# Performance work log

Measured on AMD Instinct MI355X. Metric: run time of the kernel, lower is better.

Reference implementation:

```python
import jax, jax.numpy as jnp
import numpy as np

HEADS = 16
DIM_HEAD = 64
NONCAUSAL_ATTN_LEN = 64


def setup_inputs() -> dict:
    key = jax.random.key(0)
    k1, k2, k3 = jax.random.split(key, 3)
    b, n, d = 2, 2048, 1024
    inner = HEADS * DIM_HEAD
    x = jax.random.normal(k1, (b, n, d), dtype=jnp.float32)
    mask = jnp.ones((b, n), dtype=bool)
    w_qkv = jax.random.normal(k2, (d, 3 * inner), dtype=jnp.float32) * 0.02
    w_out = jax.random.normal(k3, (inner, d), dtype=jnp.float32) * 0.02
    b_out = jnp.zeros((d,), dtype=jnp.float32)
    return {"x": x, "mask": mask, "w_qkv": w_qkv, "w_out": w_out, "b_out": b_out}


def reference(x, mask, w_qkv, w_out, b_out):
    b, n, _ = x.shape
    h, dh = HEADS, DIM_HEAD
    scale = dh ** -0.5
    qkv = x @ w_qkv                                  # [b, n, 3*h*dh]
    q, k, v = jnp.split(qkv, 3, axis=-1)
    # 'b n (h d) -> b h n d'
    reshape = lambda t: t.reshape(b, n, h, dh).transpose(0, 2, 1, 3)
    q, k, v = reshape(q), reshape(k), reshape(v)
    dots = jnp.einsum('bhid,bhjd->bhij', q, k) * scale  # [b,h,n,n]
    neg = -jnp.finfo(dots.dtype).max
    # padding mask: attend only where both query and key positions are valid
    pm = mask[:, None, :, None] & mask[:, None, None, :]
    dots = jnp.where(~pm, neg, dots)
    # causal mask (strict upper triangle), with noncausal prefix block unmasked
    cm = jnp.triu(jnp.ones((n, n), dtype=bool), k=1)
    L = NONCAUSAL_ATTN_LEN
    if L > 1:
        cm = cm.at[:L, :L].set(False)
    dots = jnp.where(cm, neg, dots)
    attn = jax.nn.softmax(dots, axis=-1)
    out = jnp.einsum('bhij,bhjd->bhid', attn, v)     # [b,h,n,dh]
    out = out.transpose(0, 2, 1, 3).reshape(b, n, h * dh)  # 'b h n d -> b n (h d)'
    return out @ w_out + b_out
```

## Files before the change

kernel.cpp:

```cpp
#include <hip/hip_runtime.h>

typedef __bf16 bf16x8 __attribute__((ext_vector_type(8)));
typedef __bf16 bf16x4 __attribute__((ext_vector_type(4)));
typedef float  f32x4  __attribute__((ext_vector_type(4)));

#define SC2 0.18033688011112042f

__device__ __forceinline__ void gload16(const void* g, void* l) {
    __builtin_amdgcn_global_load_lds(
        (const __attribute__((address_space(1))) unsigned int*)g,
        (__attribute__((address_space(3))) unsigned int*)l, 16, 0, 0);
}

__device__ __forceinline__ float max3f(float a, float b, float c) {
    return fmaxf(fmaxf(a, b), c);
}

__global__ __launch_bounds__(256) void prep_k(
    const float* __restrict__ x, const float* __restrict__ w_qkv,
    const float* __restrict__ w_out, __bf16* __restrict__ xb,
    __bf16* __restrict__ wqkvT, __bf16* __restrict__ woutT)
{
    __shared__ float tile[32][33];
    const int blk = blockIdx.x, tid = threadIdx.x;
    if (blk < 4096) {
        int i = blk * 256 + tid;
        float4 v = ((const float4*)x)[i];
        bf16x4 o;
        o[0] = (__bf16)v.x; o[1] = (__bf16)v.y; o[2] = (__bf16)v.z; o[3] = (__bf16)v.w;
        ((bf16x4*)xb)[i] = o;
        return;
    }
    const float* in; __bf16* outp; int C, t0;
    if (blk < 7168) { in = w_qkv; outp = wqkvT; C = 3072; t0 = blk - 4096; }
    else            { in = w_out; outp = woutT; C = 1024; t0 = blk - 7168; }
    const int R = 1024;
    const int tpr = C >> 5;
    const int c0 = (t0 % tpr) * 32, r0 = (t0 / tpr) * 32;
    const int tx = tid & 31, ty = tid >> 5;
#pragma unroll
    for (int p = 0; p < 4; ++p)
        tile[ty + p * 8][tx] = in[(size_t)(r0 + ty + p * 8) * C + c0 + tx];
    __syncthreads();
#pragma unroll
    for (int p = 0; p < 4; ++p)
        outp[(size_t)(c0 + ty + p * 8) * R + r0 + tx] = (__bf16)tile[tx][ty + p * 8];
}

template<int MODE, int BM>
__global__ __launch_bounds__(256) void gemm_bf16_k(
    const __bf16* __restrict__ A, const __bf16* __restrict__ Bt,
    void* __restrict__ Cout, const float* __restrict__ bias,
    int M, int N, int K)
{
    constexpr int MI = BM / 32;
    constexpr int MPX = (BM == 128) ? 4 : 8;
    constexpr int MSH = (BM == 128) ? 2 : 3;
    __shared__ __bf16 As[2][BM * 32];
    __shared__ __bf16 Bs[2][128 * 32];
    const int tid = threadIdx.x;
    const int flat = blockIdx.y * gridDim.x + blockIdx.x;
    const int xcd = flat & 7, q = flat >> 3;
    const int mi = xcd * MPX + (q & (MPX - 1));
    const int ni = q >> MSH;
    const int m0 = mi * BM, n0 = ni * 128;
    const int wave = tid >> 6, lane = tid & 63;
    const int lr = lane & 15, lk = lane >> 4;

    const int row4 = lane >> 2;
    const int sg   = (lane & 3) ^ (row4 & 3);

    const int wm = (BM == 128) ? (wave >> 1) * 64 : (wave & 1) * 32;
    const int wn = (BM == 128) ? (wave & 1) * 64 : (wave >> 1) * 64;

    f32x4 acc[MI][4] = {};

    auto stage = [&](int k0, int bufi) {
        if (BM == 128) {
#pragma unroll
            for (int c = 0; c < 2; ++c) {
                int row = c * 64 + wave * 16 + row4;
                gload16(A + (size_t)(m0 + row) * K + k0 + sg * 8,
                        (char*)&As[bufi][0] + c * 4096 + wave * 1024);
            }
        } else {
            int row = wave * 16 + row4;
            gload16(A + (size_t)(m0 + row) * K + k0 + sg * 8,
                    (char*)&As[bufi][0] + wave * 1024);
        }
#pragma unroll
        for (int c = 0; c < 2; ++c) {
            int row = c * 64 + wave * 16 + row4;
            gload16(Bt + (size_t)(n0 + row) * K + k0 + sg * 8,
                    (char*)&Bs[bufi][0] + c * 4096 + wave * 1024);
        }
    };

    const int nsteps = K >> 5;
    stage(0, 0);
    for (int s = 0; s < nsteps; ++s) {
        __syncthreads();
        if (s + 1 < nsteps) stage((s + 1) * 32, (s + 1) & 1);
        const int bufi = s & 1;

        bf16x8 af[MI], bfr[4];
#pragma unroll
        for (int i = 0; i < MI; ++i) {
            int row = wm + i * 16 + lr;
            af[i]  = *(const bf16x8*)((char*)&As[bufi][0] + row * 64 +
                                      ((lk ^ (row & 3)) << 4));
        }
#pragma unroll
        for (int j = 0; j < 4; ++j) {
            int row = wn + j * 16 + lr;
            bfr[j] = *(const bf16x8*)((char*)&Bs[bufi][0] + row * 64 +
                                      ((lk ^ (row & 3)) << 4));
        }
        __builtin_amdgcn_s_setprio(1);
#pragma unroll
        for (int i = 0; i < MI; ++i)
#pragma unroll
            for (int j = 0; j < 4; ++j)
                acc[i][j] = __builtin_amdgcn_mfma_f32_16x16x32_bf16(
                    af[i], bfr[j], acc[i][j], 0, 0, 0);
        __builtin_amdgcn_s_setprio(0);
    }

#pragma unroll
    for (int i = 0; i < MI; ++i) {
#pragma unroll
        for (int j = 0; j < 4; ++j) {
            int row0 = m0 + wm + i * 16 + lk * 4;
            int col  = n0 + wn + j * 16 + lr;
            if (MODE == 0) {
                int which = col >> 10, rem = col & 1023;
                int h = rem >> 6, dh = rem & 63;
                int bb = row0 >> 11, nn0 = row0 & 2047;
                if (which == 2) {
                    bf16x4 o;
#pragma unroll
                    for (int r = 0; r < 4; ++r) o[r] = (__bf16)acc[i][j][r];
                    size_t off = (size_t)8388608 +
                                 (((size_t)bb * 16 + h) * 64 + dh) * 2048 + nn0;
                    *(bf16x4*)((__bf16*)Cout + off) = o;
                } else {
                    float sc = (which == 0) ? SC2 : 1.f;
#pragma unroll
                    for (int r = 0; r < 4; ++r) {
                        size_t off = ((((size_t)which * 2 + bb) * 16 + h) * 2048
                                      + nn0 + r) * 64 + dh;
                        ((__bf16*)Cout)[off] = (__bf16)(acc[i][j][r] * sc);
                    }
                }
            } else {
#pragma unroll
                for (int r = 0; r < 4; ++r)
                    ((float*)Cout)[(size_t)(row0 + r) * N + col] =
                        acc[i][j][r] + bias[col];
            }
        }
    }
}

__global__ __launch_bounds__(256) void flash_attn_k(
    const __bf16* __restrict__ qkv, __bf16* __restrict__ out)
{
    __shared__ __bf16 Ks[2][64 * 64];
    __shared__ __bf16 Vt[2][64 * 64];
    __shared__ __bf16 Ps[4 * 16 * 64];

    const int g = blockIdx.x;
    const int xcd = g & 7, i = g >> 3;
    const int bh = xcd + 8 * (i & 3);
    const int qp = i >> 2;
    const int qtA = qp, qtB = 31 - qp;
    const int b = bh >> 4, h = bh & 15;
    const int wave = threadIdx.x >> 6, lane = threadIdx.x & 63;
    const int lr = lane & 15, lk = lane >> 4;

    const size_t headoff = ((size_t)b * 16 + h) * 2048 * 64;
    const __bf16* Qp  = qkv + headoff;
    const __bf16* Kp  = qkv + (size_t)4194304 + headoff;
    const __bf16* Vtp = qkv + (size_t)8388608 + headoff;

    const int row8 = lane >> 3;
    const int sg   = (lane & 7) ^ row8;

    bf16x8 qfA[2], qfB[2];
    {
        const __bf16* qa = Qp + (size_t)(qtA * 64 + wave * 16 + lr) * 64 + lk * 8;
        qfA[0] = *(const bf16x8*)(qa);
        qfA[1] = *(const bf16x8*)(qa + 32);
        const __bf16* qb = Qp + (size_t)(qtB * 64 + wave * 16 + lr) * 64 + lk * 8;
        qfB[0] = *(const bf16x8*)(qb);
        qfB[1] = *(const bf16x8*)(qb + 32);
    }

    bf16x8 ones;
#pragma unroll
    for (int j = 0; j < 8; ++j) ones[j] = (__bf16)1.0f;

    float mA = 0.f, mB = 0.f;
    f32x4 lAacc = {}, lBacc = {};
    f32x4 oA[4] = {}, oB[4] = {};

    char* PsW = (char*)Ps + wave * 2048;

    auto stage = [&](int t, int bufi) {
        const int j0 = t * 64;
#pragma unroll
        for (int c = 0; c < 2; ++c) {
            int row = c * 32 + wave * 8 + row8;
            gload16(Kp + (size_t)(j0 + row) * 64 + sg * 8,
                    (char*)&Ks[bufi][0] + c * 4096 + wave * 1024);
            gload16(Vtp + (size_t)row * 2048 + j0 + sg * 8,
                    (char*)&Vt[bufi][0] + c * 4096 + wave * 1024);
        }
    };

    auto process = [&](int bufi, const bf16x8 (&qf)[2], float& m, f32x4& lacc,
                       f32x4 (&acc_o)[4], bool diag) {
        const float nm = -m;
        f32x4 sacc[4];
#pragma unroll
        for (int nf = 0; nf < 4; ++nf) sacc[nf] = f32x4{nm, nm, nm, nm};
        __builtin_amdgcn_s_setprio(1);
#pragma unroll
        for (int nf = 0; nf < 4; ++nf) {
            int arow = nf * 16 + lr;
#pragma unroll
            for (int ks = 0; ks < 2; ++ks) {
                int kb = (arow * 128 + (ks * 32 + lk * 8) * 2) ^ ((arow & 7) << 4);
                bf16x8 kf = *(const bf16x8*)((char*)&Ks[bufi][0] + kb);
                sacc[nf] = __builtin_amdgcn_mfma_f32_16x16x32_bf16(
                    kf, qf[ks], sacc[nf], 0, 0, 0);
            }
        }
        __builtin_amdgcn_s_setprio(0);
        if (diag) {
#pragma unroll
            for (int nf = 0; nf < 4; ++nf)
#pragma unroll
                for (int r = 0; r < 4; ++r)
                    if (nf * 16 + lk * 4 + r > wave * 16 + lr)
                        sacc[nf][r] = -1e30f;
        }
        float t0 = max3f(sacc[0][0], sacc[0][1], sacc[0][2]);
        float t1 = max3f(sacc[0][3], sacc[1][0], sacc[1][1]);
        float t2 = max3f(sacc[1][2], sacc[1][3], sacc[2][0]);
        float t3 = max3f(sacc[2][1], sacc[2][2], sacc[2][3]);
        float t4 = max3f(sacc[3][0], sacc[3][1], sacc[3][2]);
        float v = fmaxf(max3f(max3f(t0, t1, t2), t3, t4), sacc[3][3]);
        v = fmaxf(v, __shfl_xor(v, 16));
        v = fmaxf(v, __shfl_xor(v, 32));
        if (__builtin_expect(__any(v > 8.f), 0)) {
            float vc = fmaxf(v, 0.f);
            float alpha = exp2f(-vc);
            m += vc;
            float a_r[4];
#pragma unroll
            for (int r = 0; r < 4; ++r) a_r[r] = __shfl(alpha, lk * 4 + r);
#pragma unroll
            for (int r = 0; r < 4; ++r) lacc[r] *= a_r[r];
#pragma unroll
            for (int nf = 0; nf < 4; ++nf)
#pragma unroll
                for (int r = 0; r < 4; ++r) {
                    acc_o[nf][r] *= a_r[r];
                    sacc[nf][r] -= vc;
                }
        }
#pragma unroll
        for (int nf = 0; nf < 4; ++nf) {
            bf16x4 o;
#pragma unroll
            for (int r = 0; r < 4; ++r) o[r] = (__bf16)exp2f(sacc[nf][r]);
            int pb = (lr * 128 + nf * 32 + lk * 8) ^ ((lr & 7) << 4);
            *(bf16x4*)(PsW + pb) = o;
        }
        __builtin_amdgcn_s_setprio(1);
#pragma unroll
        for (int ks = 0; ks < 2; ++ks) {
            int pb = (lr * 128 + ks * 64 + lk * 16) ^ ((lr & 7) << 4);
            bf16x8 pa = *(const bf16x8*)(PsW + pb);
            lacc = __builtin_amdgcn_mfma_f32_16x16x32_bf16(pa, ones, lacc, 0, 0, 0);
#pragma unroll
            for (int nf = 0; nf < 4; ++nf) {
                int d = nf * 16 + lr;
                int vb = (d * 128 + ks * 64 + lk * 16) ^ ((d & 7) << 4);
                bf16x8 vf = *(const bf16x8*)((char*)&Vt[bufi][0] + vb);
                acc_o[nf] = __builtin_amdgcn_mfma_f32_16x16x32_bf16(
                    pa, vf, acc_o[nf], 0, 0, 0);
            }
        }
        __builtin_amdgcn_s_setprio(0);
    };

    const int nt = qtB + 1;
    stage(0, 0);
    for (int t = 0; t < nt; ++t) {
        __syncthreads();
        if (t + 1 < nt) stage(t + 1, (t + 1) & 1);
        if (t <= qtA) process(t & 1, qfA, mA, lAacc, oA, t == qtA && qtA > 0);
        process(t & 1, qfB, mB, lBacc, oB, t == qtB);
    }

    float lAr[4], lBr[4];
#pragma unroll
    for (int r = 0; r < 4; ++r) {
        lAr[r] = 1.f / lAacc[r];
        lBr[r] = 1.f / lBacc[r];
    }
    const int rowbase = (b << 11) + wave * 16 + lk * 4;
    const int colbase = h * 64 + lr;
#pragma unroll
    for (int nf = 0; nf < 4; ++nf)
#pragma unroll
        for (int r = 0; r < 4; ++r) {
            out[(size_t)(rowbase + qtA * 64 + r) * 1024 + colbase + nf * 16] =
                (__bf16)(oA[nf][r] * lAr[r]);
            out[(size_t)(rowbase + qtB * 64 + r) * 1024 + colbase + nf * 16] =
                (__bf16)(oB[nf][r] * lBr[r]);
        }
}

extern "C" void kernel_launch(void* const* d_in, const int* in_sizes, int n_in,
                              void* d_out, int out_size, void* d_ws, size_t ws_size,
                              hipStream_t stream)
{
    const float* x     = (const float*)d_in[0];
    const float* w_qkv = (const float*)d_in[2];
    const float* w_out = (const float*)d_in[3];
    const float* b_out = (const float*)d_in[4];

    char* ws = (char*)d_ws;
    __bf16* xb    = (__bf16*)(ws);
    __bf16* wqkvT = (__bf16*)(ws + 8388608);
    __bf16* woutT = (__bf16*)(ws + 14680064);
    __bf16* qkvp  = (__bf16*)(ws + 16777216);
    __bf16* aout  = (__bf16*)(ws + 41943040);

    prep_k<<<8192, 256, 0, stream>>>(x, w_qkv, w_out, xb, wqkvT, woutT);

    gemm_bf16_k<0, 128><<<dim3(32, 24), 256, 0, stream>>>(
        xb, wqkvT, (void*)qkvp, nullptr, 4096, 3072, 1024);
    flash_attn_k<<<512, 256, 0, stream>>>(qkvp, aout);
    gemm_bf16_k<1, 64><<<dim3(64, 8), 256, 0, stream>>>(
        aout, woutT, (void*)d_out, b_out, 4096, 1024, 1024);
}
```

Baseline: 113.4 us.

## Replace QKV GEMM with 256x256-tile 8-wave phased pipelined kernel

Adds a dedicated QKV projection kernel that uses 256x256 output tiles, 512 threads and a 64-wide K step. The K loop is split into four phases that interleave shared-memory fragment reads, async global-to-LDS prefetch of the next tile and MFMA bursts, with swizzled LDS addressing. The larger tiles raise data reuse per byte loaded, and the phased schedule overlaps loads with math. In exchange the grid drops to 192 blocks, which may underfill the GPU, and the kernel uses 128KB LDS and many accumulator registers.

New measurement: 120.0 us. +5.8%, slower.

```diff
diff --git a/kernel.cpp b/kernel.cpp
--- a/kernel.cpp
+++ b/kernel.cpp
@@ -45,6 +45,114 @@
 #pragma unroll
     for (int p = 0; p < 4; ++p)
         outp[(size_t)(c0 + ty + p * 8) * R + r0 + tx] = (__bf16)tile[tx][ty + p * 8];
+}
+
+__global__ __launch_bounds__(512, 2) void gemm_qkv_8ph(
+    const __bf16* __restrict__ A, const __bf16* __restrict__ Bt,
+    __bf16* __restrict__ Cout)
+{
+    __shared__ __align__(16) char smem[131072];
+    const int tid = threadIdx.x;
+    const int wave = tid >> 6, lane = tid & 63;
+    const int lr = lane & 15, lk = lane >> 4;
+    const int m0 = blockIdx.x * 256, n0 = blockIdx.y * 256;
+    const int R0 = (wave >> 2) * 128;
+    const int C0 = (wave & 3) * 64;
+    const int sg   = (lane & 7) ^ (lane >> 3);
+    const int srow = wave * 8 + (lane >> 3);
+
+    f32x4 acc[8][4] = {};
+
+    auto stageA = [&](int kt, int slot) {
+        const __bf16* src = A + (size_t)(m0 + srow) * 1024 + kt * 64 + sg * 8;
+        char* dst = smem + slot * 65536 + wave * 1024;
+#pragma unroll
+        for (int c = 0; c < 4; ++c)
+            gload16(src + (size_t)c * 65536, dst + c * 8192);
+    };
+    auto stageB = [&](int kt, int slot) {
+        const __bf16* src = Bt + (size_t)(n0 + srow) * 1024 + kt * 64 + sg * 8;
+        char* dst = smem + slot * 65536 + 32768 + wave * 1024;
+#pragma unroll
+        for (int c = 0; c < 4; ++c)
+            gload16(src + (size_t)c * 65536, dst + c * 8192);
+    };
+
+    stageA(0, 0);
+    stageB(0, 0);
+    __syncthreads();
+
+    for (int t = 0; t < 16; ++t) {
+        const char* base = smem + (t & 1) * 65536;
+        const int ns = (t + 1 < 16);
+#pragma unroll
+        for (int p = 0; p < 4; ++p) {
+            const int mp = p >> 1, np = p & 1;
+            bf16x8 af[4][2], bfm[2][2];
+#pragma unroll
+            for (int i = 0; i < 4; ++i) {
+                int arow = R0 + (mp * 4 + i) * 16 + lr;
+#pragma unroll
+                for (int ks = 0; ks < 2; ++ks)
+                    af[i][ks] = *(const bf16x8*)(base + arow * 128 +
+                        (((ks << 2) | lk) ^ (arow & 7)) * 16);
+            }
+#pragma unroll
+            for (int j = 0; j < 2; ++j) {
+                int brow = C0 + (np * 2 + j) * 16 + lr;
+#pragma unroll
+                for (int ks = 0; ks < 2; ++ks)
+                    bfm[j][ks] = *(const bf16x8*)(base + 32768 + brow * 128 +
+                        (((ks << 2) | lk) ^ (brow & 7)) * 16);
+            }
+            if (ns && p == 0) stageA(t + 1, (t + 1) & 1);
+            if (ns && p == 1) stageB(t + 1, (t + 1) & 1);
+            __builtin_amdgcn_s_barrier();
+            __builtin_amdgcn_s_setprio(1);
+#pragma unroll
+            for (int i = 0; i < 4; ++i)
+#pragma unroll
+                for (int j = 0; j < 2; ++j) {
+                    int ai = mp * 4 + i, bj = np * 2 + j;
+                    acc[ai][bj] = __builtin_amdgcn_mfma_f32_16x16x32_bf16(
+                        af[i][0], bfm[j][0], acc[ai][bj], 0, 0, 0);
+                    acc[ai][bj] = __builtin_amdgcn_mfma_f32_16x16x32_bf16(
+                        af[i][1], bfm[j][1], acc[ai][bj], 0, 0, 0);
+                }
+            __builtin_amdgcn_s_setprio(0);
+            if (p == 3 && ns)
+                asm volatile("s_waitcnt vmcnt(0)" ::: "memory");
+            __builtin_amdgcn_s_barrier();
+        }
+    }
+
+#pragma unroll
+    for (int i = 0; i < 8; ++i) {
+#pragma unroll
+        for (int j = 0; j < 4; ++j) {
+            int row0 = m0 + R0 + i * 16 + lk * 4;
+            int col  = n0 + C0 + j * 16 + lr;
+            int which = col >> 10, rem = col & 1023;
+            int h = rem >> 6, dh = rem & 63;
+            int bb = row0 >> 11, nn0 = row0 & 2047;
+            if (which == 2) {
+                bf16x4 o;
+#pragma unroll
+                for (int r = 0; r < 4; ++r) o[r] = (__bf16)acc[i][j][r];
+                size_t off = (size_t)8388608 +
+                             (((size_t)bb * 16 + h) * 64 + dh) * 2048 + nn0;
+                *(bf16x4*)(Cout + off) = o;
+            } else {
+                float sc = (which == 0) ? SC2 : 1.f;
+#pragma unroll
+                for (int r = 0; r < 4; ++r) {
+                    size_t off = ((((size_t)which * 2 + bb) * 16 + h) * 2048
+                                  + nn0 + r) * 64 + dh;
+                    Cout[off] = (__bf16)(acc[i][j][r] * sc);
+                }
+            }
+        }
+    }
 }
 
 template<int MODE, int BM>
@@ -132,32 +240,10 @@
         for (int j = 0; j < 4; ++j) {
             int row0 = m0 + wm + i * 16 + lk * 4;
             int col  = n0 + wn + j * 16 + lr;
-            if (MODE == 0) {
-                int which = col >> 10, rem = col & 1023;
-                int h = rem >> 6, dh = rem & 63;
-                int bb = row0 >> 11, nn0 = row0 & 2047;
-                if (which == 2) {
-                    bf16x4 o;
-#pragma unroll
-                    for (int r = 0; r < 4; ++r) o[r] = (__bf16)acc[i][j][r];
-                    size_t off = (size_t)8388608 +
-                                 (((size_t)bb * 16 + h) * 64 + dh) * 2048 + nn0;
-                    *(bf16x4*)((__bf16*)Cout + off) = o;
-                } else {
-                    float sc = (which == 0) ? SC2 : 1.f;
-#pragma unroll
-                    for (int r = 0; r < 4; ++r) {
-                        size_t off = ((((size_t)which * 2 + bb) * 16 + h) * 2048
-                                      + nn0 + r) * 64 + dh;
-                        ((__bf16*)Cout)[off] = (__bf16)(acc[i][j][r] * sc);
-                    }
-                }
-            } else {
-#pragma unroll
-                for (int r = 0; r < 4; ++r)
-                    ((float*)Cout)[(size_t)(row0 + r) * N + col] =
-                        acc[i][j][r] + bias[col];
-            }
+#pragma unroll
+            for (int r = 0; r < 4; ++r)
+                ((float*)Cout)[(size_t)(row0 + r) * N + col] =
+                    acc[i][j][r] + bias[col];
         }
     }
 }
@@ -342,8 +428,7 @@
 
     prep_k<<<8192, 256, 0, stream>>>(x, w_qkv, w_out, xb, wqkvT, woutT);
 
-    gemm_bf16_k<0, 128><<<dim3(32, 24), 256, 0, stream>>>(
-        xb, wqkvT, (void*)qkvp, nullptr, 4096, 3072, 1024);
+    gemm_qkv_8ph<<<dim3(16, 12), 512, 0, stream>>>(xb, wqkvT, qkvp);
     flash_attn_k<<<512, 256, 0, stream>>>(qkvp, aout);
     gemm_bf16_k<1, 64><<<dim3(64, 8), 256, 0, stream>>>(
         aout, woutT, (void*)d_out, b_out, 4096, 1024, 1024);
```
